# Kernel tuning notes

Hardware: AMD Instinct MI355X
Metric: run time of the kernel (lower is better)

## Reference

```python
import jax, jax.numpy as jnp
import numpy as np
from jax import lax

B, H7, W24 = 2048, 7, 24

def _conv(x, w):
    # x: [B,Cin,H,W], w: [Cout,Cin,3,3], stride 1, SAME padding (= padding 1)
    return lax.conv_general_dilated(x, w, (1, 1), 'SAME',
                                    dimension_numbers=('NCHW', 'OIHW', 'NCHW'))

def _cell(x, h, c, Wx, bx, Wh, Wc):
    # Wx: [4H,Cin,3,3] (gates i,f,c,o fused), Wh: [4H,H,3,3], Wc: [3,1,H,Hh,Ww] peepholes (i,f,o)
    H = h.shape[1]
    g = _conv(x, Wx) + bx[None, :, None, None] + _conv(h, Wh)  # [B,4H,Hh,Ww]
    gi, gf, gc, go = jnp.split(g, 4, axis=1)
    ci = jax.nn.sigmoid(gi + c * Wc[0])
    cf = jax.nn.sigmoid(gf + c * Wc[1])
    cc = cf * c + ci * jnp.tanh(gc)
    co = jax.nn.sigmoid(go + cc * Wc[2])
    ch = co * jnp.tanh(cc)
    return ch, cc

def setup_inputs() -> dict:
    key = jax.random.key(0)
    ks = jax.random.split(key, 12)
    s = 0.05
    return {
        'input': jax.random.normal(ks[0], (B, 2, H7, W24), jnp.float32),
        'x_ex': jax.random.normal(ks[1], (B, W24), jnp.float32),
        'Wx0': jax.random.normal(ks[2], (128, 2, 3, 3), jnp.float32) * s,
        'bx0': jax.random.normal(ks[3], (128,), jnp.float32) * s,
        'Wh0': jax.random.normal(ks[4], (128, 32, 3, 3), jnp.float32) * s,
        'Wc0': jnp.zeros((3, 1, 32, H7, W24), jnp.float32),
        'Wx1': jax.random.normal(ks[5], (256, 32, 3, 3), jnp.float32) * s,
        'bx1': jax.random.normal(ks[6], (256,), jnp.float32) * s,
        'Wh1': jax.random.normal(ks[7], (256, 64, 3, 3), jnp.float32) * s,
        'Wc1': jnp.zeros((3, 1, 64, H7, W24), jnp.float32),
        'fc1_w': jax.random.normal(ks[8], (64, 64 * H7 * W24), jnp.float32) * s,
        'fc1_b': jax.random.normal(ks[9], (64,), jnp.float32) * s,
        'exfc_w': jax.random.normal(ks[10], (64, W24), jnp.float32) * s,
        'exfc_b': jax.random.normal(ks[11], (64,), jnp.float32) * s,
    }

def reference(input, x_ex, Wx0, bx0, Wh0, Wc0, Wx1, bx1, Wh1, Wc1,
              fc1_w, fc1_b, exfc_w, exfc_b):
    b = input.shape[0]
    z0 = jnp.zeros((b, 32, H7, W24), input.dtype)
    z1 = jnp.zeros((b, 64, H7, W24), input.dtype)

    def step_fn(carry, _):
        h0, c0, h1, c1 = carry
        h0, c0 = _cell(input, h0, c0, Wx0, bx0, Wh0, Wc0)
        h1, c1 = _cell(h0, h1, c1, Wx1, bx1, Wh1, Wc1)
        return (h0, c0, h1, c1), None

    (h0, c0, h1, c1), _ = lax.scan(step_fn, (z0, z0, z1, z1), None, length=7)
    # last effective-step output is the top-layer hidden state after step 7
    h1f = jax.nn.relu(h1.reshape(b, -1) @ fc1_w.T + fc1_b)
    hex_ = jax.nn.relu(x_ex @ exfc_w.T + exfc_b)
    return jnp.concatenate((h1f, hex_), axis=1)  # [B,128]
```

## Files before the change

### kernel.cpp

```cpp
#include <hip/hip_runtime.h>
#include <math.h>


typedef __bf16 bf16x8 __attribute__((ext_vector_type(8)));
typedef __bf16 bf16x4 __attribute__((ext_vector_type(4)));
typedef float  f32x4  __attribute__((ext_vector_type(4)));

__device__ __forceinline__ float sigm(float x)  { return 1.f / (1.f + __expf(-x)); }
__device__ __forceinline__ float ftanh(float x) { float e = __expf(2.f * x); return 1.f - 2.f / (e + 1.f); }

#define OFF_WP0  ((size_t)0)
#define OFF_WP1  ((size_t)81920)
#define OFF_WFC  ((size_t)524288)
#define OFF_WCP0 ((size_t)1900544)
#define OFF_WCP1 ((size_t)1932800)
#define WS_NEED  ((size_t)1997312)

#define SH0N 9360
#define SH1N 16848
#define SX2N 5376

__global__ void pack_w0(const float* __restrict__ wx0, const float* __restrict__ wh0,
                        const float* __restrict__ bx0, __bf16* __restrict__ dst) {
  int o = blockIdx.x * 256 + threadIdx.x;
  if (o >= 40960) return;
  int e = o & 7, L = (o >> 3) & 63;
  int idx = o >> 9;
  int g = idx & 3, sidx = idx >> 2;
  int s = sidx % 10, chh = sidx / 10;
  int n = g * 32 + chh * 16 + (L & 15);
  int k = s * 32 + (L >> 4) * 8 + e;
  float v = 0.f;
  if (k < 32) {
    if (k < 18) {
      int ky = k / 6, rem = k - ky * 6, kx = rem >> 1, ci = rem & 1;
      v = wx0[(n * 2 + ci) * 9 + ky * 3 + kx];
    } else if (k == 18) {
      v = bx0[n];
    }
  } else {
    int tk = k - 32, tap = tk >> 5, c = tk & 31;
    v = wh0[(n * 32 + c) * 9 + tap];
  }
  dst[o] = (__bf16)v;
}

__global__ void pack_w1(const float* __restrict__ wx1, const float* __restrict__ wh1,
                        __bf16* __restrict__ dst) {
  int o = blockIdx.x * 256 + threadIdx.x;
  if (o >= 221184) return;
  int e = o & 7, L = (o >> 3) & 63;
  int idx = o >> 9;
  int g = idx & 3, sidx = idx >> 2;
  int s = sidx % 27, chq = sidx / 27;
  int n = g * 64 + chq * 16 + (L & 15);
  int k = s * 32 + (L >> 4) * 8 + e;
  float v;
  if (k < 288) {
    int tap = k >> 5, c = k & 31;
    v = wx1[(n * 32 + c) * 9 + tap];
  } else {
    int tk = k - 288, s2 = tk >> 5, c = tk & 31, tap = s2 >> 1, hf = s2 & 1;
    v = wh1[(n * 64 + hf * 32 + c) * 9 + tap];
  }
  dst[o] = (__bf16)v;
}

__global__ void pack_wfc(const float* __restrict__ w, __bf16* __restrict__ dst) {
  int o = blockIdx.x * 256 + threadIdx.x;
  if (o >= 168 * 64 * 64) return;
  int pix = o >> 12, ch = (o >> 6) & 63, n = o & 63;
  dst[o] = (__bf16)w[n * 10752 + ch * 168 + pix];
}

__global__ void pack_wc(const float* __restrict__ wc0, const float* __restrict__ wc1,
                        __bf16* __restrict__ d0, __bf16* __restrict__ d1) {
  int o = blockIdx.x * 256 + threadIdx.x;
  if (o < 16128) d0[o] = (__bf16)wc0[o];
  else if (o < 48384) d1[o - 16128] = (__bf16)wc1[o - 16128];
}

__global__ __launch_bounds__(512, 2) void convlstm_persistent(
    const float* __restrict__ input, const float* __restrict__ x_ex,
    const __bf16* __restrict__ wp0, const __bf16* __restrict__ wp1,
    const __bf16* __restrict__ wfc2,
    const float* __restrict__ bx1,
    const __bf16* __restrict__ wcp0, const __bf16* __restrict__ wcp1,
    const float* __restrict__ fc1b,
    const float* __restrict__ exw, const float* __restrict__ exb,
    float* __restrict__ out)
{
  __shared__ __bf16 sh0[2 * SH0N];
  __shared__ __bf16 sh1[2 * SH1N];
  __shared__ __bf16 sx2[SX2N];

  const int b = blockIdx.x;
  const int t = threadIdx.x;
  const int w = t >> 6, L = t & 63;
  const int lo16 = L & 15, hi4 = L >> 4;

  {
    int* p0 = (int*)sh0;
    for (int i = t; i < SH0N; i += 512) p0[i] = 0;
    int* p1 = (int*)sh1;
    for (int i = t; i < SH1N; i += 512) p1[i] = 0;
    int* p2 = (int*)sx2;
    for (int i = t; i < SX2N / 2; i += 512) p2[i] = 0;
  }
  __syncthreads();

  if (t < 168) {
    int iy = t / 24, ix = t - iy * 24;
    __bf16* dst = sx2 + t * 32;
    for (int ky = 0; ky < 3; ++ky) {
      int y = iy + ky - 1;
      if (y < 0 || y >= 7) continue;
      for (int kx = 0; kx < 3; ++kx) {
        int x = ix + kx - 1;
        if (x < 0 || x >= 24) continue;
        int k0 = ky * 6 + kx * 2;
        dst[k0 + 0] = (__bf16)input[((b * 2 + 0) * 7 + y) * 24 + x];
        dst[k0 + 1] = (__bf16)input[((b * 2 + 1) * 7 + y) * 24 + x];
      }
    }
    dst[18] = (__bf16)1.0f;
  }

  const int chh = w & 1, m3 = w >> 1;
  const int chq = w & 3, m2 = w >> 2;
  const int ch0 = chh * 16 + lo16;
  const int ch1 = chq * 16 + lo16;

  const __bf16* w0f = wp0 + chh * 20480 + L * 8;
  const __bf16* w1f = wp1 + chq * 55296 + L * 8;

  const float bi1 = bx1[ch1], bf1 = bx1[64 + ch1];
  const float bg1 = bx1[128 + ch1], bo1 = bx1[192 + ch1];

  float c0r[3][4];
#pragma unroll
  for (int j = 0; j < 3; ++j)
#pragma unroll
    for (int r = 0; r < 4; ++r) c0r[j][r] = 0.f;

  float c1rA[3][4], c1rB[3][4];
#pragma unroll
  for (int j = 0; j < 3; ++j)
#pragma unroll
    for (int r = 0; r < 4; ++r) { c1rA[j][r] = 0.f; c1rB[j][r] = 0.f; }

  __syncthreads();

#pragma unroll 1
  for (int st = 0; st < 7; ++st) {
    const __bf16* h0r = sh0 + (st & 1) * SH0N;
    __bf16*       h0w = sh0 + ((st + 1) & 1) * SH0N;
    const __bf16* h1r = sh1 + (st & 1) * SH1N;
    __bf16*       h1w = sh1 + ((st + 1) & 1) * SH1N;

    {
      const int tb = m3 * 3;
      const int ntq = (m3 == 3) ? 2 : 3;
      int b0h[3], b0x[3];
#pragma unroll
      for (int j = 0; j < 3; ++j) {
        int pr = (tb + j) * 16 + lo16;
        if (pr > 167) pr = 167;
        int iy = pr / 24, ix = pr - iy * 24;
        b0h[j] = (iy * 26 + ix) * 40;
        b0x[j] = pr * 32 + hi4 * 8;
      }
      f32x4 a0[4][3];
#pragma unroll
      for (int g = 0; g < 4; ++g)
#pragma unroll
        for (int j = 0; j < 3; ++j) a0[g][j] = (f32x4){0.f, 0.f, 0.f, 0.f};

      auto loadA0 = [&](int s, bf16x8* af) {
        if (s == 0) {
#pragma unroll
          for (int j = 0; j < 3; ++j) af[j] = *(const bf16x8*)(sx2 + b0x[j]);
        } else {
          int tap = s - 1, ky = tap / 3, kx = tap - ky * 3;
          int toff = (ky * 26 + kx) * 40 + hi4 * 8;
#pragma unroll
          for (int j = 0; j < 3; ++j) af[j] = *(const bf16x8*)(h0r + b0h[j] + toff);
        }
      };
      auto loadB0 = [&](int s, bf16x8* bc) {
#pragma unroll
        for (int g = 0; g < 4; ++g)
          bc[g] = *(const bf16x8*)(w0f + (s * 4 + g) * 512);
      };
      auto mfma0 = [&](bf16x8* af, bf16x8* bc) {
#pragma unroll
        for (int j = 0; j < 3; ++j)
#pragma unroll
          for (int g = 0; g < 4; ++g)
            a0[g][j] = __builtin_amdgcn_mfma_f32_16x16x32_bf16(af[j], bc[g], a0[g][j], 0, 0, 0);
      };

      bf16x8 afA[3], afB[3], bcA[4], bcB[4];
      loadA0(0, afA); loadB0(0, bcA);
      loadA0(1, afB); loadB0(1, bcB);
#pragma unroll 1
      for (int s = 0; s < 10; s += 2) {
        mfma0(afA, bcA);
        int s2 = (s + 2 < 10) ? s + 2 : 9;
        loadA0(s2, afA); loadB0(s2, bcA);
        mfma0(afB, bcB);
        int s3 = (s + 3 < 10) ? s + 3 : 9;
        loadA0(s3, afB); loadB0(s3, bcB);
      }

#pragma unroll
      for (int j = 0; j < 3; ++j) {
        int p0 = (tb + j) * 16 + hi4 * 4;
        if (j < ntq && p0 < 168) {
          const __bf16* wpp = wcp0 + ch0 * 168 + p0;
          bf16x4 w_i = *(const bf16x4*)(wpp);
          bf16x4 w_f = *(const bf16x4*)(wpp + 5376);
          bf16x4 w_o = *(const bf16x4*)(wpp + 10752);
#pragma unroll
          for (int r = 0; r < 4; ++r) {
            int p = p0 + r;
            float c = c0r[j][r];
            float gi = a0[0][j][r];
            float gf = a0[1][j][r];
            float gc = a0[2][j][r];
            float go = a0[3][j][r];
            float ig = sigm(gi + c * (float)w_i[r]);
            float fg = sigm(gf + c * (float)w_f[r]);
            float cn = fg * c + ig * ftanh(gc);
            float og = sigm(go + cn * (float)w_o[r]);
            float hn = og * ftanh(cn);
            c0r[j][r] = cn;
            int iy = p / 24, ix = p - iy * 24;
            h0w[((iy + 1) * 26 + ix + 1) * 40 + ch0] = (__bf16)hn;
          }
        }
      }
    }
    __syncthreads();

    auto l1pass = [&](int tb, int ntp, float (&c1)[3][4]) {
      int b1h0[3], b1h1[3];
#pragma unroll
      for (int j = 0; j < 3; ++j) {
        int pr = (tb + j) * 16 + lo16;
        if (pr > 167) pr = 167;
        int iy = pr / 24, ix = pr - iy * 24;
        b1h0[j] = (iy * 26 + ix) * 40;
        b1h1[j] = (iy * 26 + ix) * 72;
      }
      f32x4 a1[4][3];
      {
        const float binit[4] = {bi1, bf1, bg1, bo1};
#pragma unroll
        for (int g = 0; g < 4; ++g)
#pragma unroll
          for (int j = 0; j < 3; ++j)
            a1[g][j] = (f32x4){binit[g], binit[g], binit[g], binit[g]};
      }

      auto loadA1 = [&](int s, bf16x8* af) {
        if (s < 9) {
          int ky = s / 3, kx = s - ky * 3;
          int toff = (ky * 26 + kx) * 40 + hi4 * 8;
#pragma unroll
          for (int j = 0; j < 3; ++j) af[j] = *(const bf16x8*)(h0w + b1h0[j] + toff);
        } else {
          int t2 = s - 9, tap = t2 >> 1, hf = t2 & 1;
          int ky = tap / 3, kx = tap - ky * 3;
          int toff = (ky * 26 + kx) * 72 + hf * 32 + hi4 * 8;
#pragma unroll
          for (int j = 0; j < 3; ++j) af[j] = *(const bf16x8*)(h1r + b1h1[j] + toff);
        }
      };
      auto loadB1 = [&](int s, bf16x8* bc) {
#pragma unroll
        for (int g = 0; g < 4; ++g)
          bc[g] = *(const bf16x8*)(w1f + (s * 4 + g) * 512);
      };
      auto mfma1 = [&](bf16x8* af, bf16x8* bc) {
#pragma unroll
        for (int j = 0; j < 3; ++j) {
          if (j < ntp) {
#pragma unroll
            for (int g = 0; g < 4; ++g)
              a1[g][j] = __builtin_amdgcn_mfma_f32_16x16x32_bf16(af[j], bc[g], a1[g][j], 0, 0, 0);
          }
        }
      };

      bf16x8 afA[3], afB[3], bcA[4], bcB[4];
      loadA1(0, afA); loadB1(0, bcA);
      loadA1(1, afB); loadB1(1, bcB);
#pragma unroll 1
      for (int s = 0; s < 26; s += 2) {
        mfma1(afA, bcA);
        int s2 = (s + 2 < 27) ? s + 2 : 26;
        loadA1(s2, afA); loadB1(s2, bcA);
        mfma1(afB, bcB);
        int s3 = (s + 3 < 27) ? s + 3 : 26;
        loadA1(s3, afB); loadB1(s3, bcB);
      }
      mfma1(afA, bcA);

#pragma unroll
      for (int j = 0; j < 3; ++j) {
        int p0 = (tb + j) * 16 + hi4 * 4;
        if (j < ntp && p0 < 168) {
          const __bf16* wpp = wcp1 + ch1 * 168 + p0;
          bf16x4 w_i = *(const bf16x4*)(wpp);
          bf16x4 w_f = *(const bf16x4*)(wpp + 10752);
          bf16x4 w_o = *(const bf16x4*)(wpp + 21504);
#pragma unroll
          for (int r = 0; r < 4; ++r) {
            int p = p0 + r;
            float c = c1[j][r];
            float gi = a1[0][j][r];
            float gf = a1[1][j][r];
            float gc = a1[2][j][r];
            float go = a1[3][j][r];
            float ig = sigm(gi + c * (float)w_i[r]);
            float fg = sigm(gf + c * (float)w_f[r]);
            float cn = fg * c + ig * ftanh(gc);
            float og = sigm(go + cn * (float)w_o[r]);
            float hn = og * ftanh(cn);
            c1[j][r] = cn;
            int iy = p / 24, ix = p - iy * 24;
            h1w[((iy + 1) * 26 + ix + 1) * 72 + ch1] = (__bf16)hn;
          }
        }
      }
    };
    l1pass(m2 * 6,     3,                    c1rA);
    l1pass(m2 * 6 + 3, (m2 == 1) ? 2 : 3,    c1rB);
  }
  __syncthreads();

  {
    const __bf16* h1f = sh1 + SH1N;
    const int o = t & 3, pg = t >> 2;
    float part[16];
#pragma unroll
    for (int q = 0; q < 16; ++q) part[q] = 0.f;
#pragma unroll 1
    for (int jj = 0; jj < 2; ++jj) {
      int p = pg + 128 * jj;
      if (p < 168) {
        int iy = p / 24, ix = p - iy * 24;
        const __bf16* hrow = h1f + ((iy + 1) * 26 + ix + 1) * 72;
        const __bf16* wrow = wfc2 + (size_t)p * 4096 + o * 16;
        for (int ch = 0; ch < 64; ++ch) {
          float hv = (float)hrow[ch];
          bf16x8 wv0 = *(const bf16x8*)(wrow + ch * 64);
          bf16x8 wv1 = *(const bf16x8*)(wrow + ch * 64 + 8);
#pragma unroll
          for (int q = 0; q < 8; ++q) {
            part[q] += hv * (float)wv0[q];
            part[8 + q] += hv * (float)wv1[q];
          }
        }
      }
    }
    float* sacc = (float*)sh0;
#pragma unroll
    for (int q = 0; q < 16; ++q) sacc[pg * 64 + o * 16 + q] = part[q];
    __syncthreads();
    if (t < 64) {
      float s = fc1b[t];
      for (int pg2 = 0; pg2 < 128; ++pg2) s += sacc[pg2 * 64 + t];
      out[(size_t)b * 128 + t] = fmaxf(s, 0.f);
    } else if (t < 128) {
      int j = t - 64;
      float s = exb[j];
      for (int k = 0; k < 24; ++k) s += x_ex[b * 24 + k] * exw[j * 24 + k];
      out[(size_t)b * 128 + 64 + j] = fmaxf(s, 0.f);
    }
  }
}

extern "C" void kernel_launch(void* const* d_in, const int* in_sizes, int n_in,
                              void* d_out, int out_size, void* d_ws, size_t ws_size,
                              hipStream_t stream) {
  const float* input = (const float*)d_in[0];
  const float* x_ex  = (const float*)d_in[1];
  const float* Wx0   = (const float*)d_in[2];
  const float* bx0   = (const float*)d_in[3];
  const float* Wh0   = (const float*)d_in[4];
  const float* Wc0   = (const float*)d_in[5];
  const float* Wx1   = (const float*)d_in[6];
  const float* bx1   = (const float*)d_in[7];
  const float* Wh1   = (const float*)d_in[8];
  const float* Wc1   = (const float*)d_in[9];
  const float* fc1w  = (const float*)d_in[10];
  const float* fc1b  = (const float*)d_in[11];
  const float* exw   = (const float*)d_in[12];
  const float* exb   = (const float*)d_in[13];
  (void)in_sizes; (void)n_in;

  if (ws_size < WS_NEED) {
    hipMemsetAsync(d_out, 0, (size_t)out_size * 4, stream);
    return;
  }

  char* ws = (char*)d_ws;
  __bf16* wp0  = (__bf16*)(ws + OFF_WP0);
  __bf16* wp1  = (__bf16*)(ws + OFF_WP1);
  __bf16* wfc2 = (__bf16*)(ws + OFF_WFC);
  __bf16* wcp0 = (__bf16*)(ws + OFF_WCP0);
  __bf16* wcp1 = (__bf16*)(ws + OFF_WCP1);

  pack_w0<<<160, 256, 0, stream>>>(Wx0, Wh0, bx0, wp0);
  pack_w1<<<864, 256, 0, stream>>>(Wx1, Wh1, wp1);
  pack_wfc<<<2688, 256, 0, stream>>>(fc1w, wfc2);
  pack_wc<<<189, 256, 0, stream>>>(Wc0, Wc1, wcp0, wcp1);

  convlstm_persistent<<<2048, 512, 0, stream>>>(
      input, x_ex, wp0, wp1, wfc2, bx1, wcp0, wcp1, fc1b, exw, exb,
      (float*)d_out);
}
```

Baseline: 2.243 ms.

## Widen ConvLSTM blocks to 12 waves, repartition tiles, add wave-reduced FC

Raises the block size from 512 to 768 threads and reassigns MFMA tiles: layer 0 now runs 2 pixel tiles per wave and layer 1 runs 4 tiles per wave in a single pass instead of two passes of 3. The layer-1 A-fragment loads drop the double buffer, the MFMA sections are wrapped in s_setprio, and the FC reduction becomes a wave shuffle reduction with nontemporal weight loads, so the final LDS sum covers 12 entries instead of 128. The aim is more waves per block to hide latency and a cheaper FC reduction. In exchange, per-thread register pressure rises under the 768×3 launch bound, and the single-buffered A loads add load latency on the critical path.

Result: slower. 3.004 ms (+34.0%).

```diff
diff --git a/kernel.cpp b/kernel.cpp
--- a/kernel.cpp
+++ b/kernel.cpp
@@ -8,6 +8,9 @@
 
 __device__ __forceinline__ float sigm(float x)  { return 1.f / (1.f + __expf(-x)); }
 __device__ __forceinline__ float ftanh(float x) { float e = __expf(2.f * x); return 1.f - 2.f / (e + 1.f); }
+__device__ __forceinline__ bf16x8 ntld8(const __bf16* p) {
+  return __builtin_nontemporal_load((const bf16x8*)p);
+}
 
 #define OFF_WP0  ((size_t)0)
 #define OFF_WP1  ((size_t)81920)
@@ -80,7 +83,7 @@
   else if (o < 48384) d1[o - 16128] = (__bf16)wc1[o - 16128];
 }
 
-__global__ __launch_bounds__(512, 2) void convlstm_persistent(
+__global__ __launch_bounds__(768, 3) void convlstm_persistent(
     const float* __restrict__ input, const float* __restrict__ x_ex,
     const __bf16* __restrict__ wp0, const __bf16* __restrict__ wp1,
     const __bf16* __restrict__ wfc2,
@@ -101,11 +104,11 @@
 
   {
     int* p0 = (int*)sh0;
-    for (int i = t; i < SH0N; i += 512) p0[i] = 0;
+    for (int i = t; i < SH0N; i += 768) p0[i] = 0;
     int* p1 = (int*)sh1;
-    for (int i = t; i < SH1N; i += 512) p1[i] = 0;
+    for (int i = t; i < SH1N; i += 768) p1[i] = 0;
     int* p2 = (int*)sx2;
-    for (int i = t; i < SX2N / 2; i += 512) p2[i] = 0;
+    for (int i = t; i < SX2N / 2; i += 768) p2[i] = 0;
   }
   __syncthreads();
 
@@ -126,8 +129,8 @@
     dst[18] = (__bf16)1.0f;
   }
 
-  const int chh = w & 1, m3 = w >> 1;
-  const int chq = w & 3, m2 = w >> 2;
+  const int chh = w & 1, m6 = w >> 1;
+  const int chq = w & 3, m3 = w >> 2;
   const int ch0 = chh * 16 + lo16;
   const int ch1 = chq * 16 + lo16;
 
@@ -137,17 +140,17 @@
   const float bi1 = bx1[ch1], bf1 = bx1[64 + ch1];
   const float bg1 = bx1[128 + ch1], bo1 = bx1[192 + ch1];
 
-  float c0r[3][4];
-#pragma unroll
-  for (int j = 0; j < 3; ++j)
+  float c0r[2][4];
+#pragma unroll
+  for (int j = 0; j < 2; ++j)
 #pragma unroll
     for (int r = 0; r < 4; ++r) c0r[j][r] = 0.f;
 
-  float c1rA[3][4], c1rB[3][4];
-#pragma unroll
-  for (int j = 0; j < 3; ++j)
-#pragma unroll
-    for (int r = 0; r < 4; ++r) { c1rA[j][r] = 0.f; c1rB[j][r] = 0.f; }
+  float c1r[4][4];
+#pragma unroll
+  for (int j = 0; j < 4; ++j)
+#pragma unroll
+    for (int r = 0; r < 4; ++r) c1r[j][r] = 0.f;
 
   __syncthreads();
 
@@ -159,32 +162,32 @@
     __bf16*       h1w = sh1 + ((st + 1) & 1) * SH1N;
 
     {
-      const int tb = m3 * 3;
-      const int ntq = (m3 == 3) ? 2 : 3;
-      int b0h[3], b0x[3];
-#pragma unroll
-      for (int j = 0; j < 3; ++j) {
+      const int tb = m6 * 2;
+      const int ntq = (m6 == 5) ? 1 : 2;
+      int b0h[2], b0x[2];
+#pragma unroll
+      for (int j = 0; j < 2; ++j) {
         int pr = (tb + j) * 16 + lo16;
         if (pr > 167) pr = 167;
         int iy = pr / 24, ix = pr - iy * 24;
         b0h[j] = (iy * 26 + ix) * 40;
         b0x[j] = pr * 32 + hi4 * 8;
       }
-      f32x4 a0[4][3];
+      f32x4 a0[4][2];
 #pragma unroll
       for (int g = 0; g < 4; ++g)
 #pragma unroll
-        for (int j = 0; j < 3; ++j) a0[g][j] = (f32x4){0.f, 0.f, 0.f, 0.f};
+        for (int j = 0; j < 2; ++j) a0[g][j] = (f32x4){0.f, 0.f, 0.f, 0.f};
 
       auto loadA0 = [&](int s, bf16x8* af) {
         if (s == 0) {
 #pragma unroll
-          for (int j = 0; j < 3; ++j) af[j] = *(const bf16x8*)(sx2 + b0x[j]);
+          for (int j = 0; j < 2; ++j) af[j] = *(const bf16x8*)(sx2 + b0x[j]);
         } else {
           int tap = s - 1, ky = tap / 3, kx = tap - ky * 3;
           int toff = (ky * 26 + kx) * 40 + hi4 * 8;
 #pragma unroll
-          for (int j = 0; j < 3; ++j) af[j] = *(const bf16x8*)(h0r + b0h[j] + toff);
+          for (int j = 0; j < 2; ++j) af[j] = *(const bf16x8*)(h0r + b0h[j] + toff);
         }
       };
       auto loadB0 = [&](int s, bf16x8* bc) {
@@ -194,27 +197,31 @@
       };
       auto mfma0 = [&](bf16x8* af, bf16x8* bc) {
 #pragma unroll
-        for (int j = 0; j < 3; ++j)
+        for (int j = 0; j < 2; ++j)
 #pragma unroll
           for (int g = 0; g < 4; ++g)
             a0[g][j] = __builtin_amdgcn_mfma_f32_16x16x32_bf16(af[j], bc[g], a0[g][j], 0, 0, 0);
       };
 
-      bf16x8 afA[3], afB[3], bcA[4], bcB[4];
+      bf16x8 afA[2], afB[2], bcA[4], bcB[4];
       loadA0(0, afA); loadB0(0, bcA);
       loadA0(1, afB); loadB0(1, bcB);
 #pragma unroll 1
       for (int s = 0; s < 10; s += 2) {
+        __builtin_amdgcn_s_setprio(1);
         mfma0(afA, bcA);
+        __builtin_amdgcn_s_setprio(0);
         int s2 = (s + 2 < 10) ? s + 2 : 9;
         loadA0(s2, afA); loadB0(s2, bcA);
+        __builtin_amdgcn_s_setprio(1);
         mfma0(afB, bcB);
+        __builtin_amdgcn_s_setprio(0);
         int s3 = (s + 3 < 10) ? s + 3 : 9;
         loadA0(s3, afB); loadB0(s3, bcB);
       }
 
 #pragma unroll
-      for (int j = 0; j < 3; ++j) {
+      for (int j = 0; j < 2; ++j) {
         int p0 = (tb + j) * 16 + hi4 * 4;
         if (j < ntq && p0 < 168) {
           const __bf16* wpp = wcp0 + ch0 * 168 + p0;
@@ -243,23 +250,25 @@
     }
     __syncthreads();
 
-    auto l1pass = [&](int tb, int ntp, float (&c1)[3][4]) {
-      int b1h0[3], b1h1[3];
-#pragma unroll
-      for (int j = 0; j < 3; ++j) {
+    {
+      const int tb = m3 * 4;
+      const int ntp = (m3 == 2) ? 3 : 4;
+      int b1h0[4], b1h1[4];
+#pragma unroll
+      for (int j = 0; j < 4; ++j) {
         int pr = (tb + j) * 16 + lo16;
         if (pr > 167) pr = 167;
         int iy = pr / 24, ix = pr - iy * 24;
         b1h0[j] = (iy * 26 + ix) * 40;
         b1h1[j] = (iy * 26 + ix) * 72;
       }
-      f32x4 a1[4][3];
+      f32x4 a1[4][4];
       {
         const float binit[4] = {bi1, bf1, bg1, bo1};
 #pragma unroll
         for (int g = 0; g < 4; ++g)
 #pragma unroll
-          for (int j = 0; j < 3; ++j)
+          for (int j = 0; j < 4; ++j)
             a1[g][j] = (f32x4){binit[g], binit[g], binit[g], binit[g]};
       }
 
@@ -268,13 +277,13 @@
           int ky = s / 3, kx = s - ky * 3;
           int toff = (ky * 26 + kx) * 40 + hi4 * 8;
 #pragma unroll
-          for (int j = 0; j < 3; ++j) af[j] = *(const bf16x8*)(h0w + b1h0[j] + toff);
+          for (int j = 0; j < 4; ++j) af[j] = *(const bf16x8*)(h0w + b1h0[j] + toff);
         } else {
           int t2 = s - 9, tap = t2 >> 1, hf = t2 & 1;
           int ky = tap / 3, kx = tap - ky * 3;
           int toff = (ky * 26 + kx) * 72 + hf * 32 + hi4 * 8;
 #pragma unroll
-          for (int j = 0; j < 3; ++j) af[j] = *(const bf16x8*)(h1r + b1h1[j] + toff);
+          for (int j = 0; j < 4; ++j) af[j] = *(const bf16x8*)(h1r + b1h1[j] + toff);
         }
       };
       auto loadB1 = [&](int s, bf16x8* bc) {
@@ -284,7 +293,7 @@
       };
       auto mfma1 = [&](bf16x8* af, bf16x8* bc) {
 #pragma unroll
-        for (int j = 0; j < 3; ++j) {
+        for (int j = 0; j < 4; ++j) {
           if (j < ntp) {
 #pragma unroll
             for (int g = 0; g < 4; ++g)
@@ -293,22 +302,27 @@
         }
       };
 
-      bf16x8 afA[3], afB[3], bcA[4], bcB[4];
-      loadA1(0, afA); loadB1(0, bcA);
-      loadA1(1, afB); loadB1(1, bcB);
+      bf16x8 af[4], bcA[4], bcB[4];
+      loadA1(0, af); loadB1(0, bcA); loadB1(1, bcB);
 #pragma unroll 1
       for (int s = 0; s < 26; s += 2) {
-        mfma1(afA, bcA);
-        int s2 = (s + 2 < 27) ? s + 2 : 26;
-        loadA1(s2, afA); loadB1(s2, bcA);
-        mfma1(afB, bcB);
-        int s3 = (s + 3 < 27) ? s + 3 : 26;
-        loadA1(s3, afB); loadB1(s3, bcB);
-      }
-      mfma1(afA, bcA);
-
-#pragma unroll
-      for (int j = 0; j < 3; ++j) {
+        __builtin_amdgcn_s_setprio(1);
+        mfma1(af, bcA);
+        __builtin_amdgcn_s_setprio(0);
+        loadB1((s + 2 < 27) ? s + 2 : 26, bcA);
+        loadA1(s + 1, af);
+        __builtin_amdgcn_s_setprio(1);
+        mfma1(af, bcB);
+        __builtin_amdgcn_s_setprio(0);
+        loadB1((s + 3 < 27) ? s + 3 : 26, bcB);
+        loadA1((s + 2 < 27) ? s + 2 : 26, af);
+      }
+      __builtin_amdgcn_s_setprio(1);
+      mfma1(af, bcA);
+      __builtin_amdgcn_s_setprio(0);
+
+#pragma unroll
+      for (int j = 0; j < 4; ++j) {
         int p0 = (tb + j) * 16 + hi4 * 4;
         if (j < ntp && p0 < 168) {
           const __bf16* wpp = wcp1 + ch1 * 168 + p0;
@@ -318,7 +332,7 @@
 #pragma unroll
           for (int r = 0; r < 4; ++r) {
             int p = p0 + r;
-            float c = c1[j][r];
+            float c = c1r[j][r];
             float gi = a1[0][j][r];
             float gf = a1[1][j][r];
             float gc = a1[2][j][r];
@@ -328,15 +342,13 @@
             float cn = fg * c + ig * ftanh(gc);
             float og = sigm(go + cn * (float)w_o[r]);
             float hn = og * ftanh(cn);
-            c1[j][r] = cn;
+            c1r[j][r] = cn;
             int iy = p / 24, ix = p - iy * 24;
             h1w[((iy + 1) * 26 + ix + 1) * 72 + ch1] = (__bf16)hn;
           }
         }
       }
-    };
-    l1pass(m2 * 6,     3,                    c1rA);
-    l1pass(m2 * 6 + 3, (m2 == 1) ? 2 : 3,    c1rB);
+    }
   }
   __syncthreads();
 
@@ -346,32 +358,46 @@
     float part[16];
 #pragma unroll
     for (int q = 0; q < 16; ++q) part[q] = 0.f;
+    if (pg < 168) {
+      int iy = pg / 24, ix = pg - iy * 24;
+      const __bf16* hrow = h1f + ((iy + 1) * 26 + ix + 1) * 72;
+      const __bf16* wrow = wfc2 + (size_t)pg * 4096 + o * 16;
 #pragma unroll 1
-    for (int jj = 0; jj < 2; ++jj) {
-      int p = pg + 128 * jj;
-      if (p < 168) {
-        int iy = p / 24, ix = p - iy * 24;
-        const __bf16* hrow = h1f + ((iy + 1) * 26 + ix + 1) * 72;
-        const __bf16* wrow = wfc2 + (size_t)p * 4096 + o * 16;
-        for (int ch = 0; ch < 64; ++ch) {
-          float hv = (float)hrow[ch];
-          bf16x8 wv0 = *(const bf16x8*)(wrow + ch * 64);
-          bf16x8 wv1 = *(const bf16x8*)(wrow + ch * 64 + 8);
+      for (int c8 = 0; c8 < 8; ++c8) {
+        bf16x8 hv = *(const bf16x8*)(hrow + c8 * 8);
+#pragma unroll
+        for (int u = 0; u < 8; ++u) {
+          float hvf = (float)hv[u];
+          const __bf16* wp = wrow + (c8 * 8 + u) * 64;
+          bf16x8 wv0 = ntld8(wp);
+          bf16x8 wv1 = ntld8(wp + 8);
 #pragma unroll
           for (int q = 0; q < 8; ++q) {
-            part[q] += hv * (float)wv0[q];
-            part[8 + q] += hv * (float)wv1[q];
+            part[q] += hvf * (float)wv0[q];
+            part[8 + q] += hvf * (float)wv1[q];
           }
         }
       }
     }
-    float* sacc = (float*)sh0;
-#pragma unroll
-    for (int q = 0; q < 16; ++q) sacc[pg * 64 + o * 16 + q] = part[q];
+#pragma unroll
+    for (int q = 0; q < 16; ++q) {
+      float v = part[q];
+      v += __shfl_xor(v, 4);
+      v += __shfl_xor(v, 8);
+      v += __shfl_xor(v, 16);
+      v += __shfl_xor(v, 32);
+      part[q] = v;
+    }
+    float* sacc = (float*)sx2;
+    if (L < 4) {
+#pragma unroll
+      for (int q = 0; q < 16; ++q) sacc[w * 64 + L * 16 + q] = part[q];
+    }
     __syncthreads();
     if (t < 64) {
       float s = fc1b[t];
-      for (int pg2 = 0; pg2 < 128; ++pg2) s += sacc[pg2 * 64 + t];
+#pragma unroll
+      for (int w2 = 0; w2 < 12; ++w2) s += sacc[w2 * 64 + t];
       out[(size_t)b * 128 + t] = fmaxf(s, 0.f);
     } else if (t < 128) {
       int j = t - 64;
@@ -418,7 +444,7 @@
   pack_wfc<<<2688, 256, 0, stream>>>(fc1w, wfc2);
   pack_wc<<<189, 256, 0, stream>>>(Wc0, Wc1, wcp0, wcp1);
 
-  convlstm_persistent<<<2048, 512, 0, stream>>>(
+  convlstm_persistent<<<2048, 768, 0, stream>>>(
       input, x_ex, wp0, wp1, wfc2, bx1, wcp0, wcp1, fc1b, exw, exb,
       (float*)d_out);
 }
```
